# Performance work log

Measured on AMD Instinct MI355X. Metric: run time of the kernel, lower is better.

## Reference

```python
import jax, jax.numpy as jnp
import numpy as np

# NF4 codebook (bitsandbytes normal-float-4 quantile values)
NF4 = jnp.array([-1.0, -0.6961928009986877, -0.5250730514526367, -0.39491748809814453,
                 -0.28444138169288635, -0.18477343022823334, -0.09105003625154495, 0.0,
                 0.07958029955625534, 0.16093020141124725, 0.24611230194568634,
                 0.33791524171829224, 0.44070982933044434, 0.5626170039176941,
                 0.7229568362236023, 1.0], dtype=jnp.float32)
BLOCK = 64          # bnb default quantization block size
SCALING = 32.0 / 16.0  # lora_alpha / r


def setup_inputs() -> dict:
    key = jax.random.key(0)
    k1, k2, k3, k4, k5 = jax.random.split(key, 5)
    B, S, DIN, DOUT, R = 4, 2048, 4096, 4096, 16
    x = jax.random.normal(k1, (B, S, DIN), dtype=jnp.float32)
    w_codes = jax.random.randint(k2, (DOUT, DIN), 0, 16, dtype=jnp.int32)
    absmax = jax.random.uniform(k3, (DOUT, DIN // BLOCK), dtype=jnp.float32)
    lora_A_w = jax.random.normal(k4, (R, DIN), dtype=jnp.float32) * (1.0 / np.sqrt(DIN))
    lora_B_w = jax.random.normal(k5, (DOUT, R), dtype=jnp.float32) * 0.02
    return {"x": x, "w_codes": w_codes, "absmax": absmax,
            "lora_A_w": lora_A_w, "lora_B_w": lora_B_w}


def _dequant_nf4(w_codes, absmax):
    # codes -> codebook values, scaled per contiguous block of BLOCK elements per row
    dout, din = w_codes.shape
    w = NF4[w_codes].reshape(dout, din // BLOCK, BLOCK) * absmax[:, :, None]
    return w.reshape(dout, din)  # [out, in] float32


def reference(x, w_codes, absmax, lora_A_w, lora_B_w):
    w = _dequant_nf4(w_codes, absmax)                      # [out, in]
    logits = jnp.einsum('bsd,od->bso', x, w)               # base 4-bit path
    a = jnp.einsum('bsd,rd->bsr', x, lora_A_w)             # [b,s,r]
    lora = jnp.einsum('bsr,or->bso', a, lora_B_w) * SCALING
    return logits + lora
```

## Files before the change

kernel.cpp:

```cpp
#include <hip/hip_runtime.h>

#define GLOBAL_AS __attribute__((address_space(1)))
#define LDS_AS    __attribute__((address_space(3)))

typedef short bf16x8 __attribute__((ext_vector_type(8)));
typedef float f32x4  __attribute__((ext_vector_type(4)));

#define M_DIM 8192
#define N_DIM 4096
#define K_DIM 4096
#define R_DIM 16
#define KAUG  4224

__constant__ float NF4C[16] = {
    -1.0f, -0.6961928009986877f, -0.5250730514526367f, -0.39491748809814453f,
    -0.28444138169288635f, -0.18477343022823334f, -0.09105003625154495f, 0.0f,
    0.07958029955625534f, 0.16093020141124725f, 0.24611230194568634f,
    0.33791524171829224f, 0.44070982933044434f, 0.5626170039176941f,
    0.7229568362236023f, 1.0f};

__device__ __forceinline__ unsigned short f2bf(float f) {
    unsigned int u = __float_as_uint(f);
    u += 0x7fffu + ((u >> 16) & 1u);
    return (unsigned short)(u >> 16);
}

__global__ __launch_bounds__(256) void prep_x_kernel(
        const float4* __restrict__ x4, const float4* __restrict__ A4,
        unsigned short* __restrict__ xb) {
    const int tid = threadIdx.x;
    const int wave = tid >> 6, lane = tid & 63;
    const int m = blockIdx.x * 4 + wave;
    const float4* xrow = x4 + (size_t)m * 1024;
    unsigned short* xbrow = xb + (size_t)m * KAUG;
    float acc[16];
#pragma unroll
    for (int r = 0; r < 16; ++r) acc[r] = 0.0f;
    for (int ii = 0; ii < 16; ++ii) {
        const int k4 = lane + ii * 64;
        float4 xv = xrow[k4];
        ushort4 o;
        o.x = f2bf(xv.x); o.y = f2bf(xv.y); o.z = f2bf(xv.z); o.w = f2bf(xv.w);
        *(ushort4*)(xbrow + k4 * 4) = o;
#pragma unroll
        for (int r = 0; r < 16; ++r) {
            float4 av = A4[r * 1024 + k4];
            acc[r] += xv.x * av.x + xv.y * av.y + xv.z * av.z + xv.w * av.w;
        }
    }
#pragma unroll
    for (int r = 0; r < 16; ++r) {
#pragma unroll
        for (int off = 32; off; off >>= 1)
            acc[r] += __shfl_xor(acc[r], off, 64);
    }
    float v = 0.0f;
#pragma unroll
    for (int r = 0; r < 16; ++r) v = (lane == r) ? acc[r] : v;
    xbrow[K_DIM + lane]      = (lane < 16) ? f2bf(v) : (unsigned short)0;
    xbrow[K_DIM + 64 + lane] = 0;
}

__global__ __launch_bounds__(256) void dequant_kernel(
        const int4* __restrict__ codes4, const float* __restrict__ absmax,
        const float* __restrict__ loraB, unsigned short* __restrict__ wq) {
    const int idx = blockIdx.x * 256 + threadIdx.x;
    const int n = idx >> 10;
    const int k4 = idx & 1023;
    const float am = absmax[n * 64 + (k4 >> 4)];
    int4 c = codes4[idx];
    ushort4 o;
    o.x = f2bf(NF4C[c.x] * am);
    o.y = f2bf(NF4C[c.y] * am);
    o.z = f2bf(NF4C[c.z] * am);
    o.w = f2bf(NF4C[c.w] * am);
    *(ushort4*)(wq + (size_t)n * KAUG + k4 * 4) = o;
    if (k4 < 32) {
        ushort4 l = {0, 0, 0, 0};
        if (k4 < 4) {
            const int c0 = k4 * 4;
            l.x = f2bf(2.0f * loraB[n * R_DIM + c0 + 0]);
            l.y = f2bf(2.0f * loraB[n * R_DIM + c0 + 1]);
            l.z = f2bf(2.0f * loraB[n * R_DIM + c0 + 2]);
            l.w = f2bf(2.0f * loraB[n * R_DIM + c0 + 3]);
        }
        *(ushort4*)(wq + (size_t)n * KAUG + K_DIM + k4 * 4) = l;
    }
}

#define STG(gptr, ldsoff)                                                   \
    __builtin_amdgcn_global_load_lds((const GLOBAL_AS void*)(gptr),         \
                                     (LDS_AS void*)(smem + (ldsoff)), 16, 0, 0)
#define STAGE_A(d, kh, kt) do {                                             \
    STG(gA + (size_t)(kt) * 64 + (kh) * 32,                                 \
        (d) * 16384 + (kh) * 8192 + wave * 512);                            \
    STG(gA + (size_t)128 * KAUG + (size_t)(kt) * 64 + (kh) * 32,            \
        (d) * 16384 + (kh) * 8192 + 4096 + wave * 512); } while (0)
#define STAGE_B(d, kh, kt) do {                                             \
    STG(gB + (size_t)(kt) * 64 + (kh) * 32,                                 \
        32768 + (d) * 16384 + (kh) * 8192 + wave * 512);                    \
    STG(gB + (size_t)128 * KAUG + (size_t)(kt) * 64 + (kh) * 32,            \
        32768 + (d) * 16384 + (kh) * 8192 + 4096 + wave * 512); } while (0)
#define NOPX ((void)0)
#define VMCNT6 asm volatile("s_waitcnt vmcnt(6)" ::: "memory")
#define VMCNT0 asm volatile("s_waitcnt vmcnt(0)" ::: "memory")

#define PHASE(d, kh, mig, STAGE_STMT, VM_STMT) do {                         \
    bf16x8 af[4];                                                           \
    _Pragma("unroll")                                                       \
    for (int i_ = 0; i_ < 4; ++i_)                                          \
        af[i_] = *(const bf16x8*)(smem + (d) * 16384 + (kh) * 8192 + aoff + \
                                  ((mig) * 4 + i_) * 512);                  \
    if ((mig) == 0) {                                                       \
        _Pragma("unroll")                                                   \
        for (int j_ = 0; j_ < 4; ++j_)                                      \
            bfr[j_] = *(const bf16x8*)(smem + (d) * 16384 + (kh) * 8192 +   \
                                       boff + j_ * 512);                    \
    }                                                                       \
    STAGE_STMT;                                                             \
    __builtin_amdgcn_s_barrier();                                           \
    asm volatile("s_waitcnt lgkmcnt(0)" ::: "memory");                      \
    __builtin_amdgcn_sched_barrier(0);                                      \
    __builtin_amdgcn_s_setprio(1);                                          \
    _Pragma("unroll")                                                       \
    for (int i_ = 0; i_ < 4; ++i_)                                          \
        _Pragma("unroll")                                                   \
        for (int j_ = 0; j_ < 4; ++j_)                                      \
            acc[(mig) * 4 + i_][j_] = __builtin_amdgcn_mfma_f32_16x16x32_bf16( \
                af[i_], bfr[j_], acc[(mig) * 4 + i_][j_], 0, 0, 0);         \
    __builtin_amdgcn_s_setprio(0);                                          \
    VM_STMT;                                                                \
    __builtin_amdgcn_s_barrier();                                           \
} while (0)

__global__ __launch_bounds__(512) void gemm_kernel(
        const unsigned short* __restrict__ xb,
        const unsigned short* __restrict__ wq,
        float* __restrict__ out) {
    __shared__ __align__(16) unsigned short smem[65536];
    const int tid = threadIdx.x;
    const int wave = tid >> 6, lane = tid & 63;

    const int bid = blockIdx.y * 16 + blockIdx.x;
    const int swz = (bid & 7) * 64 + (bid >> 3);
    const int m0 = (swz >> 4) * 256;
    const int n0 = (swz & 15) * 256;

    const int schunk = ((lane & 3) ^ ((lane >> 3) & 3)) * 8;
    const unsigned short* gA =
        xb + (size_t)(m0 + wave * 16 + (lane >> 2)) * KAUG + schunk;
    const unsigned short* gB =
        wq + (size_t)(n0 + wave * 16 + (lane >> 2)) * KAUG + schunk;

    const int wr = wave >> 2, wc = wave & 3;
    const int fm = lane & 15, q = lane >> 4;
    const int rk = (q ^ ((fm >> 1) & 3)) * 8;
    const int aoff = wr * 4096 + fm * 32 + rk;
    const int boff = 32768 + wc * 2048 + fm * 32 + rk;

    f32x4 acc[8][4] = {};
    bf16x8 bfr[4];

    STAGE_A(0, 0, 0); STAGE_B(0, 0, 0); STAGE_A(0, 1, 0); STAGE_B(0, 1, 0);
    STAGE_B(1, 0, 1); STAGE_A(1, 0, 1); STAGE_B(1, 1, 1);
    VMCNT6;
    __builtin_amdgcn_s_barrier();

#pragma unroll 1
    for (int kt = 0; kt < 64; kt += 2) {
        PHASE(0, 0, 0, STAGE_A(1, 1, kt + 1), NOPX);
        PHASE(0, 0, 1, STAGE_B(0, 0, kt + 2), NOPX);
        PHASE(0, 1, 0, STAGE_A(0, 0, kt + 2), NOPX);
        PHASE(0, 1, 1, STAGE_B(0, 1, kt + 2), VMCNT6);
        PHASE(1, 0, 0, STAGE_A(0, 1, kt + 2), NOPX);
        PHASE(1, 0, 1, STAGE_B(1, 0, kt + 3), NOPX);
        PHASE(1, 1, 0, STAGE_A(1, 0, kt + 3), NOPX);
        PHASE(1, 1, 1, STAGE_B(1, 1, kt + 3), VMCNT6);
    }
    PHASE(0, 0, 0, STAGE_A(1, 1, 65), NOPX);
    PHASE(0, 0, 1, NOPX, NOPX);
    PHASE(0, 1, 0, NOPX, NOPX);
    PHASE(0, 1, 1, NOPX, VMCNT0);
    PHASE(1, 0, 0, NOPX, NOPX);
    PHASE(1, 0, 1, NOPX, NOPX);
    PHASE(1, 1, 0, NOPX, NOPX);
    PHASE(1, 1, 1, NOPX, NOPX);

    const int col0 = n0 + wc * 64 + fm;
    const int row0 = m0 + wr * 128 + q * 4;
#pragma unroll
    for (int mi = 0; mi < 8; ++mi)
#pragma unroll
        for (int ni = 0; ni < 4; ++ni)
#pragma unroll
            for (int r = 0; r < 4; ++r)
                out[(size_t)(row0 + mi * 16 + r) * N_DIM + col0 + ni * 16] =
                    acc[mi][ni][r];
}

extern "C" void kernel_launch(void* const* d_in, const int* in_sizes, int n_in,
                              void* d_out, int out_size, void* d_ws, size_t ws_size,
                              hipStream_t stream) {
    const float* x      = (const float*)d_in[0];
    const int*   codes  = (const int*)d_in[1];
    const float* absmax = (const float*)d_in[2];
    const float* loraA  = (const float*)d_in[3];
    const float* loraB  = (const float*)d_in[4];
    float* out = (float*)d_out;

    unsigned short* xb = (unsigned short*)d_ws;
    unsigned short* wq = xb + (size_t)M_DIM * KAUG;

    prep_x_kernel<<<M_DIM / 4, 256, 0, stream>>>((const float4*)x,
                                                 (const float4*)loraA, xb);
    dequant_kernel<<<(N_DIM * K_DIM / 4) / 256, 256, 0, stream>>>(
        (const int4*)codes, absmax, loraB, wq);

    dim3 grid(N_DIM / 256, M_DIM / 256);
    gemm_kernel<<<grid, 512, 0, stream>>>(xb, wq, out);
}
```

Baseline: 590.2 us.

## Fold LoRA product into dequantized weight instead of augmenting K dimension

Precomputes W + 2*B*A per weight element inside the dequant kernel, so the GEMM runs over K=4096 instead of an augmented K=4224 and prep_x becomes a plain fp32-to-bf16 conversion. This removes the extra K-tile iterations in the GEMM and the per-row LoRA-A reduction from prep_x, at the cost of a 16-term dot product per weight element during dequant. Rounding changes slightly because the small LoRA contribution is now added before bf16 rounding of the weight.

```diff
diff --git a/kernel.cpp b/kernel.cpp
--- a/kernel.cpp
+++ b/kernel.cpp
@@ -10,7 +10,6 @@
 #define N_DIM 4096
 #define K_DIM 4096
 #define R_DIM 16
-#define KAUG  4224
 
 __constant__ float NF4C[16] = {
     -1.0f, -0.6961928009986877f, -0.5250730514526367f, -0.39491748809814453f,
@@ -26,66 +25,40 @@
 }
 
 __global__ __launch_bounds__(256) void prep_x_kernel(
-        const float4* __restrict__ x4, const float4* __restrict__ A4,
-        unsigned short* __restrict__ xb) {
-    const int tid = threadIdx.x;
-    const int wave = tid >> 6, lane = tid & 63;
-    const int m = blockIdx.x * 4 + wave;
-    const float4* xrow = x4 + (size_t)m * 1024;
-    unsigned short* xbrow = xb + (size_t)m * KAUG;
-    float acc[16];
-#pragma unroll
-    for (int r = 0; r < 16; ++r) acc[r] = 0.0f;
-    for (int ii = 0; ii < 16; ++ii) {
-        const int k4 = lane + ii * 64;
-        float4 xv = xrow[k4];
-        ushort4 o;
-        o.x = f2bf(xv.x); o.y = f2bf(xv.y); o.z = f2bf(xv.z); o.w = f2bf(xv.w);
-        *(ushort4*)(xbrow + k4 * 4) = o;
-#pragma unroll
-        for (int r = 0; r < 16; ++r) {
-            float4 av = A4[r * 1024 + k4];
-            acc[r] += xv.x * av.x + xv.y * av.y + xv.z * av.z + xv.w * av.w;
-        }
-    }
-#pragma unroll
-    for (int r = 0; r < 16; ++r) {
-#pragma unroll
-        for (int off = 32; off; off >>= 1)
-            acc[r] += __shfl_xor(acc[r], off, 64);
-    }
-    float v = 0.0f;
-#pragma unroll
-    for (int r = 0; r < 16; ++r) v = (lane == r) ? acc[r] : v;
-    xbrow[K_DIM + lane]      = (lane < 16) ? f2bf(v) : (unsigned short)0;
-    xbrow[K_DIM + 64 + lane] = 0;
+        const float4* __restrict__ x4, unsigned short* __restrict__ xb) {
+    const int idx = blockIdx.x * 256 + threadIdx.x;
+    float4 v = x4[idx];
+    ushort4 o;
+    o.x = f2bf(v.x); o.y = f2bf(v.y); o.z = f2bf(v.z); o.w = f2bf(v.w);
+    *(ushort4*)(xb + (size_t)idx * 4) = o;
 }
 
 __global__ __launch_bounds__(256) void dequant_kernel(
         const int4* __restrict__ codes4, const float* __restrict__ absmax,
-        const float* __restrict__ loraB, unsigned short* __restrict__ wq) {
+        const float4* __restrict__ loraB4, const float4* __restrict__ A4,
+        unsigned short* __restrict__ wq) {
     const int idx = blockIdx.x * 256 + threadIdx.x;
     const int n = idx >> 10;
     const int k4 = idx & 1023;
     const float am = absmax[n * 64 + (k4 >> 4)];
     int4 c = codes4[idx];
+    float4 b[4];
+#pragma unroll
+    for (int j = 0; j < 4; ++j) b[j] = loraB4[n * 4 + j];
+    float bax = 0.f, bay = 0.f, baz = 0.f, baw = 0.f;
+#pragma unroll
+    for (int r = 0; r < 16; ++r) {
+        const float br = (r & 2) ? ((r & 1) ? b[r >> 2].w : b[r >> 2].z)
+                                 : ((r & 1) ? b[r >> 2].y : b[r >> 2].x);
+        float4 av = A4[r * 1024 + k4];
+        bax += br * av.x; bay += br * av.y; baz += br * av.z; baw += br * av.w;
+    }
     ushort4 o;
-    o.x = f2bf(NF4C[c.x] * am);
-    o.y = f2bf(NF4C[c.y] * am);
-    o.z = f2bf(NF4C[c.z] * am);
-    o.w = f2bf(NF4C[c.w] * am);
-    *(ushort4*)(wq + (size_t)n * KAUG + k4 * 4) = o;
-    if (k4 < 32) {
-        ushort4 l = {0, 0, 0, 0};
-        if (k4 < 4) {
-            const int c0 = k4 * 4;
-            l.x = f2bf(2.0f * loraB[n * R_DIM + c0 + 0]);
-            l.y = f2bf(2.0f * loraB[n * R_DIM + c0 + 1]);
-            l.z = f2bf(2.0f * loraB[n * R_DIM + c0 + 2]);
-            l.w = f2bf(2.0f * loraB[n * R_DIM + c0 + 3]);
-        }
-        *(ushort4*)(wq + (size_t)n * KAUG + K_DIM + k4 * 4) = l;
-    }
+    o.x = f2bf(NF4C[c.x] * am + 2.0f * bax);
+    o.y = f2bf(NF4C[c.y] * am + 2.0f * bay);
+    o.z = f2bf(NF4C[c.z] * am + 2.0f * baz);
+    o.w = f2bf(NF4C[c.w] * am + 2.0f * baw);
+    *(ushort4*)(wq + (size_t)n * K_DIM + k4 * 4) = o;
 }
 
 #define STG(gptr, ldsoff)                                                   \
@@ -94,12 +67,12 @@
 #define STAGE_A(d, kh, kt) do {                                             \
     STG(gA + (size_t)(kt) * 64 + (kh) * 32,                                 \
         (d) * 16384 + (kh) * 8192 + wave * 512);                            \
-    STG(gA + (size_t)128 * KAUG + (size_t)(kt) * 64 + (kh) * 32,            \
+    STG(gA + (size_t)128 * K_DIM + (size_t)(kt) * 64 + (kh) * 32,           \
         (d) * 16384 + (kh) * 8192 + 4096 + wave * 512); } while (0)
 #define STAGE_B(d, kh, kt) do {                                             \
     STG(gB + (size_t)(kt) * 64 + (kh) * 32,                                 \
         32768 + (d) * 16384 + (kh) * 8192 + wave * 512);                    \
-    STG(gB + (size_t)128 * KAUG + (size_t)(kt) * 64 + (kh) * 32,            \
+    STG(gB + (size_t)128 * K_DIM + (size_t)(kt) * 64 + (kh) * 32,           \
         32768 + (d) * 16384 + (kh) * 8192 + 4096 + wave * 512); } while (0)
 #define NOPX ((void)0)
 #define VMCNT6 asm volatile("s_waitcnt vmcnt(6)" ::: "memory")
@@ -148,9 +121,9 @@
 
     const int schunk = ((lane & 3) ^ ((lane >> 3) & 3)) * 8;
     const unsigned short* gA =
-        xb + (size_t)(m0 + wave * 16 + (lane >> 2)) * KAUG + schunk;
+        xb + (size_t)(m0 + wave * 16 + (lane >> 2)) * K_DIM + schunk;
     const unsigned short* gB =
-        wq + (size_t)(n0 + wave * 16 + (lane >> 2)) * KAUG + schunk;
+        wq + (size_t)(n0 + wave * 16 + (lane >> 2)) * K_DIM + schunk;
 
     const int wr = wave >> 2, wc = wave & 3;
     const int fm = lane & 15, q = lane >> 4;
@@ -167,7 +140,7 @@
     __builtin_amdgcn_s_barrier();
 
 #pragma unroll 1
-    for (int kt = 0; kt < 64; kt += 2) {
+    for (int kt = 0; kt < 62; kt += 2) {
         PHASE(0, 0, 0, STAGE_A(1, 1, kt + 1), NOPX);
         PHASE(0, 0, 1, STAGE_B(0, 0, kt + 2), NOPX);
         PHASE(0, 1, 0, STAGE_A(0, 0, kt + 2), NOPX);
@@ -177,7 +150,7 @@
         PHASE(1, 1, 0, STAGE_A(1, 0, kt + 3), NOPX);
         PHASE(1, 1, 1, STAGE_B(1, 1, kt + 3), VMCNT6);
     }
-    PHASE(0, 0, 0, STAGE_A(1, 1, 65), NOPX);
+    PHASE(0, 0, 0, STAGE_A(1, 1, 63), NOPX);
     PHASE(0, 0, 1, NOPX, NOPX);
     PHASE(0, 1, 0, NOPX, NOPX);
     PHASE(0, 1, 1, NOPX, VMCNT0);
@@ -209,12 +182,12 @@
     float* out = (float*)d_out;
 
     unsigned short* xb = (unsigned short*)d_ws;
-    unsigned short* wq = xb + (size_t)M_DIM * KAUG;
+    unsigned short* wq = xb + (size_t)M_DIM * K_DIM;
 
-    prep_x_kernel<<<M_DIM / 4, 256, 0, stream>>>((const float4*)x,
-                                                 (const float4*)loraA, xb);
+    prep_x_kernel<<<(M_DIM * K_DIM / 4) / 256, 256, 0, stream>>>(
+        (const float4*)x, xb);
     dequant_kernel<<<(N_DIM * K_DIM / 4) / 256, 256, 0, stream>>>(
-        (const int4*)codes, absmax, loraB, wq);
+        (const int4*)codes, absmax, (const float4*)loraB, (const float4*)loraA, wq);
 
     dim3 grid(N_DIM / 256, M_DIM / 256);
     gemm_kernel<<<grid, 512, 0, stream>>>(xb, wq, out);
```

Result: faster. 545.4 us (-7.6%).
